# Performance work log

Hardware: AMD Instinct MI355X
Metric: run time of the kernel (lower is better)

The kernel has to match this reference:

```python
import jax, jax.numpy as jnp
import numpy as np
import math

FACTOR = 1

def setup_inputs() -> dict:
    key = jax.random.key(0)
    kq, kk, kv = jax.random.split(key, 3)
    B, H, L, E = 8, 8, 1024, 512
    queries = jax.random.normal(kq, (B, H, L, E), dtype=jnp.float32)
    keys = jax.random.normal(kk, (B, H, L, E), dtype=jnp.float32)
    values = jax.random.normal(kv, (B, H, L, E), dtype=jnp.float32)
    return {"queries": queries, "keys": keys, "values": values}

def _time_delay_agg_full(values, corr):
    # values: [B,H,C,Len], corr: [B,H,C,Len]  (C = seq positions, Len = feature dim here)
    length = values.shape[-1]
    top_k = int(FACTOR * math.log(length))
    weights, delay = jax.lax.top_k(corr, top_k)          # [B,H,C,k]
    tmp_corr = jax.nn.softmax(weights, axis=-1)          # [B,H,C,k]
    # gather from values.repeat(...,2) at init_index + delay  ==  circular gather mod length
    idx = (jnp.arange(length)[None, None, None, None, :] + delay[..., None]) % length  # [B,H,C,k,Len]
    gathered = jnp.take_along_axis(values[:, :, :, None, :], idx, axis=-1)             # [B,H,C,k,Len]
    return jnp.einsum('bhckl,bhck->bhcl', gathered, tmp_corr)

def reference(queries, keys, values):
    B, H, L, E = queries.shape
    S = values.shape[2]
    # L == S in this setup, so pad/slice branches are no-ops; keep slice for fidelity
    values = values[:, :, :L, :]
    keys = keys[:, :, :L, :]
    q_fft = jnp.fft.fft(queries, axis=-1)
    k_fft = jnp.fft.fft(keys, axis=-1)
    res = q_fft * jnp.conj(k_fft)
    # torch.fft.irfft(res, n=E) trims the complex input to E//2+1 before inverse; numpy/jax do the same
    corr = jnp.fft.irfft(res, n=E, axis=-1).astype(queries.dtype)  # [B,H,L,E]
    V = _time_delay_agg_full(values, corr)
    return V, jnp.transpose(corr, (0, 3, 1, 2))
```

## Files before the change

kernel.cpp:

```cpp
#include <hip/hip_runtime.h>
#include <math.h>


#define TOPK 6
#define LGKM0 asm volatile("s_waitcnt lgkmcnt(0)" ::: "memory")

__device__ __forceinline__ float2 cmul(float2 a, float2 b) {
  return make_float2(fmaf(a.x, b.x, -(a.y * b.y)), fmaf(a.x, b.y, a.y * b.x));
}
__device__ __forceinline__ float2 cadd(float2 a, float2 b) { return make_float2(a.x + b.x, a.y + b.y); }
__device__ __forceinline__ float2 csub(float2 a, float2 b) { return make_float2(a.x - b.x, a.y - b.y); }
__device__ __forceinline__ float2 mnegi(float2 v) { return make_float2(v.y, -v.x); }

__device__ __forceinline__ unsigned bf16rne(float x) {
  unsigned t = __float_as_uint(x);
  return (t + 0x7FFFu + ((t >> 16) & 1u)) >> 16;
}

__device__ __forceinline__ unsigned wave_umax64(unsigned x) {
#define DPPMAX(ctrl)                                                          \
  {                                                                           \
    unsigned t = (unsigned)__builtin_amdgcn_update_dpp(0, (int)x, ctrl, 0xf,  \
                                                       0xf, true);            \
    x = t > x ? t : x;                                                        \
  }
  DPPMAX(0x111)
  DPPMAX(0x112)
  DPPMAX(0x114)
  DPPMAX(0x118)
  DPPMAX(0x142)
  DPPMAX(0x143)
#undef DPPMAX
  return (unsigned)__builtin_amdgcn_readlane((int)x, 63);
}

__device__ __forceinline__ void radix8(float2 y[8]) {
  float2 p0 = cadd(y[0], y[4]), p1 = csub(y[0], y[4]);
  float2 p2 = cadd(y[2], y[6]), p3 = csub(y[2], y[6]);
  float2 q0 = cadd(y[1], y[5]), q1 = csub(y[1], y[5]);
  float2 q2 = cadd(y[3], y[7]), q3 = csub(y[3], y[7]);
  float2 mp3 = mnegi(p3), mq3 = mnegi(q3);
  float2 E0 = cadd(p0, p2), E2 = csub(p0, p2);
  float2 E1 = cadd(p1, mp3), E3 = csub(p1, mp3);
  float2 O0 = cadd(q0, q2), O2 = csub(q0, q2);
  float2 O1 = cadd(q1, mq3), O3 = csub(q1, mq3);
  const float RT = 0.70710678118654752440f;
  float2 T1 = make_float2(RT * (O1.x + O1.y), RT * (O1.y - O1.x));
  float2 T2 = mnegi(O2);
  float2 T3 = make_float2(RT * (O3.y - O3.x), -RT * (O3.x + O3.y));
  y[0] = cadd(E0, O0); y[4] = csub(E0, O0);
  y[1] = cadd(E1, T1); y[5] = csub(E1, T1);
  y[2] = cadd(E2, T2); y[6] = csub(E2, T2);
  y[3] = cadd(E3, T3); y[7] = csub(E3, T3);
}

__device__ __forceinline__ void twiddle8(float2 y[8], float2 w) {
  float2 wp = w;
  y[1] = cmul(y[1], wp);
  wp = cmul(wp, w); y[2] = cmul(y[2], wp);
  wp = cmul(wp, w); y[3] = cmul(y[3], wp);
  wp = cmul(wp, w); y[4] = cmul(y[4], wp);
  wp = cmul(wp, w); y[5] = cmul(y[5], wp);
  wp = cmul(wp, w); y[6] = cmul(y[6], wp);
  wp = cmul(wp, w); y[7] = cmul(y[7], wp);
}

__device__ __forceinline__ void fft512t(float2 y[8], float* zx, float* zy,
                                        int u, float2 w512u, float2 w64n0) {
  const int f0 = u >> 3, n0 = u & 7;
  radix8(y);
  twiddle8(y, w512u);
#pragma unroll
  for (int r = 0; r < 8; ++r) { int s = 72 * r + u; zx[s] = y[r].x; zy[s] = y[r].y; }
  LGKM0;
#pragma unroll
  for (int j = 0; j < 8; ++j) {
    int s = 72 * f0 + 8 * j + n0;
    y[j] = make_float2(zx[s], zy[s]);
  }
  radix8(y);
  twiddle8(y, w64n0);
  LGKM0;
#pragma unroll
  for (int g = 0; g < 8; ++g) {
    int s = 72 * f0 + 8 * g + (n0 ^ g);
    zx[s] = y[g].x; zy[s] = y[g].y;
  }
  LGKM0;
#pragma unroll
  for (int j = 0; j < 8; ++j) {
    int s = 72 * f0 + 8 * n0 + (j ^ n0);
    y[j] = make_float2(zx[s], zy[s]);
  }
  radix8(y);
}

__global__ __launch_bounds__(512, 4) void autoagg_kernel(
    const float* __restrict__ q, const float* __restrict__ kk,
    const float* __restrict__ v, float* __restrict__ outV,
    float* __restrict__ outC) {
  __shared__ float zscr[8 * 1152];
  __shared__ unsigned short tile[512 * 36];
  const int tid = threadIdx.x;
  const int u = tid & 63;
  const int w = tid >> 6;
  const int bid = blockIdx.x;
  float* zx = zscr + w * 1152;
  float* zy = zx + 576;

  const int f0 = u >> 3, n0 = u & 7;
  const int base = f0 + (n0 << 3);

  const float N2PI = -6.28318530717958647692f;
  float s_, c_;
  __sincosf(N2PI * (float)u * (1.f / 512.f), &s_, &c_);
  const float2 w512u = make_float2(c_, s_);
  __sincosf(N2PI * (float)n0 * (1.f / 64.f), &s_, &c_);
  const float2 w64n0 = make_float2(c_, s_);

#pragma unroll 1
  for (int p = 0; p < 4; ++p) {
    const int row = (bid << 5) + (p << 3) + w;
    const int rowU = __builtin_amdgcn_readfirstlane(row);
    const float* qrow = q + (size_t)rowU * 512;
    const float* krow = kk + (size_t)rowU * 512;
    const float* vrow = v + (size_t)rowU * 512;

    float2 y[8];
#pragma unroll
    for (int m = 0; m < 8; ++m)
      y[m] = make_float2(qrow[u + (m << 6)], krow[u + (m << 6)]);

    fft512t(y, zx, zy, u, w512u, w64n0);

    LGKM0;
#pragma unroll
    for (int r = 0; r < 8; ++r) {
      int s = 72 * r + (n0 << 3) + f0;
      zx[s] = y[r].x; zy[s] = y[r].y;
    }
    LGKM0;
    const float SCL = 1.f / 2048.f;
#pragma unroll
    for (int m = 0; m < 8; ++m) {
      int fA = (m << 6) | u;
      int fB = (512 - fA) & 511;
      int sA = 72 * m + (f0 << 3) + n0;
      int sB = 72 * (fB >> 6) + (((fB >> 3) & 7) << 3) + (fB & 7);
      float Ax = zx[sA], Ay = zy[sA];
      float Bx = zx[sB], By = zy[sB];
      float sx = Ax + Bx, sy = Ay - By;
      float dx = Ax - Bx, dy = Ay + By;
      y[m] = make_float2((sx * dy - sy * dx) * SCL,
                         -fmaf(sx, dx, sy * dy) * SCL);
    }

    fft512t(y, zx, zy, u, w512u, w64n0);

    const int col = (p << 3) | w;
#pragma unroll
    for (int r = 0; r < 8; ++r)
      tile[(base + (r << 6)) * 36 + col] = (unsigned short)bf16rne(y[r].x);

    unsigned key[8];
#pragma unroll
    for (int r = 0; r < 8; ++r) {
      unsigned bb = __float_as_uint(y[r].x);
      unsigned sgn = (unsigned)((int)bb >> 31);
      unsigned mono = bb ^ (sgn | 0x80000000u);
      key[r] = (mono & 0xFFFFFE00u) | (unsigned)(511 - (base + (r << 6)));
    }
    float w0 = 0.f, tw[TOPK]; int dly[TOPK];
#pragma unroll
    for (int it = 0; it < TOPK; ++it) {
      unsigned km = key[0];
#pragma unroll
      for (int i = 1; i < 8; ++i) km = key[i] > km ? key[i] : km;
      unsigned kmax = wave_umax64(km);
      unsigned mb = kmax & 0xFFFFFE00u;
      unsigned vb = (mb & 0x80000000u) ? (mb ^ 0x80000000u) : ~mb;
      float val = __uint_as_float(vb);
      if (it == 0) w0 = val;
      tw[it] = __expf(val - w0);
      dly[it] = 511 - (int)(kmax & 0x1FFu);
#pragma unroll
      for (int i = 0; i < 8; ++i) if (key[i] == kmax) key[i] = 0u;
    }
    float ssum = 0.f;
#pragma unroll
    for (int it = 0; it < TOPK; ++it) ssum += tw[it];
    const float inv = 1.f / ssum;

    float V[8] = {0.f, 0.f, 0.f, 0.f, 0.f, 0.f, 0.f, 0.f};
#pragma unroll
    for (int it = 0; it < TOPK; ++it) {
      const float twk = tw[it] * inv;
      const int d = dly[it];
#pragma unroll
      for (int i = 0; i < 8; ++i)
        V[i] = fmaf(twk, vrow[(base + (i << 6) + d) & 511], V[i]);
    }

    LGKM0;
#pragma unroll
    for (int i = 0; i < 8; ++i)
      zx[76 * i + 9 * n0 + f0] = V[i];
    LGKM0;
    float vt[8];
#pragma unroll
    for (int j = 0; j < 8; ++j)
      vt[j] = zx[76 * f0 + 9 * n0 + j];
    LGKM0;
    float4* ov = (float4*)(outV + (size_t)rowU * 512 + (u << 3));
    ov[0] = make_float4(vt[0], vt[1], vt[2], vt[3]);
    ov[1] = make_float4(vt[4], vt[5], vt[6], vt[7]);
  }

  __syncthreads();
  const int b9 = bid >> 8;
  const int h9 = (bid >> 5) & 7;
  const int l0 = (bid & 31) << 5;
#pragma unroll
  for (int round = 0; round < 8; ++round) {
    int e = (round << 6) + (tid >> 3);
    int lq = (tid & 7) << 2;
    const unsigned short* tr = tile + e * 36 + lq;
    float4 tv = make_float4(__uint_as_float((unsigned)tr[0] << 16),
                            __uint_as_float((unsigned)tr[1] << 16),
                            __uint_as_float((unsigned)tr[2] << 16),
                            __uint_as_float((unsigned)tr[3] << 16));
    *(float4*)(outC + (((size_t)b9 * 512 + e) * 8 + h9) * 1024 + l0 + lq) = tv;
  }
}

extern "C" void kernel_launch(void* const* d_in, const int* in_sizes, int n_in,
                              void* d_out, int out_size, void* d_ws, size_t ws_size,
                              hipStream_t stream) {
  const float* q = (const float*)d_in[0];
  const float* k = (const float*)d_in[1];
  const float* v = (const float*)d_in[2];
  float* outV = (float*)d_out;
  float* outC = (float*)d_out + (size_t)8 * 8 * 1024 * 512;
  dim3 grid(65536 / 32), block(512);
  hipLaunchKernelGGL(autoagg_kernel, grid, block, 0, stream, q, k, v, outV, outC);
}
```

Measured before the change: 230.6 us.

## Recompute twiddles in FFT, drop explicit LDS waits, raise occupancy bound

Recomputes the FFT twiddle factors inside each FFT call with __sincosf instead of keeping them live across the loop. Explicit s_waitcnt lgkmcnt(0) waits are replaced with plain compiler memory barriers. The launch bounds move from 4 to 5 blocks per CU to push register usage down. The bf16 tile readback uses one 8-byte LDS load instead of four 2-byte loads. These aim to cut register pressure and LDS wait stalls, at the cost of extra transcendental work and relying on the compiler to insert correct LDS waits within a wave.

Result: no change. 233.0 us (+1.0%).

```diff
diff --git a/kernel.cpp b/kernel.cpp
--- a/kernel.cpp
+++ b/kernel.cpp
@@ -3,7 +3,7 @@
 
 
 #define TOPK 6
-#define LGKM0 asm volatile("s_waitcnt lgkmcnt(0)" ::: "memory")
+#define CBAR asm volatile("" ::: "memory")
 
 __device__ __forceinline__ float2 cmul(float2 a, float2 b) {
   return make_float2(fmaf(a.x, b.x, -(a.y * b.y)), fmaf(a.x, b.y, a.y * b.x));
@@ -66,27 +66,31 @@
 }
 
 __device__ __forceinline__ void fft512t(float2 y[8], float* zx, float* zy,
-                                        int u, float2 w512u, float2 w64n0) {
+                                        int u) {
   const int f0 = u >> 3, n0 = u & 7;
+  const float N2PI = -6.28318530717958647692f;
+  float s_, c_;
   radix8(y);
-  twiddle8(y, w512u);
+  __sincosf(N2PI * (float)u * (1.f / 512.f), &s_, &c_);
+  twiddle8(y, make_float2(c_, s_));
 #pragma unroll
   for (int r = 0; r < 8; ++r) { int s = 72 * r + u; zx[s] = y[r].x; zy[s] = y[r].y; }
-  LGKM0;
+  CBAR;
 #pragma unroll
   for (int j = 0; j < 8; ++j) {
     int s = 72 * f0 + 8 * j + n0;
     y[j] = make_float2(zx[s], zy[s]);
   }
   radix8(y);
-  twiddle8(y, w64n0);
-  LGKM0;
+  __sincosf(N2PI * (float)n0 * (1.f / 64.f), &s_, &c_);
+  twiddle8(y, make_float2(c_, s_));
+  CBAR;
 #pragma unroll
   for (int g = 0; g < 8; ++g) {
     int s = 72 * f0 + 8 * g + (n0 ^ g);
     zx[s] = y[g].x; zy[s] = y[g].y;
   }
-  LGKM0;
+  CBAR;
 #pragma unroll
   for (int j = 0; j < 8; ++j) {
     int s = 72 * f0 + 8 * n0 + (j ^ n0);
@@ -95,7 +99,7 @@
   radix8(y);
 }
 
-__global__ __launch_bounds__(512, 4) void autoagg_kernel(
+__global__ __launch_bounds__(512, 5) void autoagg_kernel(
     const float* __restrict__ q, const float* __restrict__ kk,
     const float* __restrict__ v, float* __restrict__ outV,
     float* __restrict__ outC) {
@@ -111,13 +115,6 @@
   const int f0 = u >> 3, n0 = u & 7;
   const int base = f0 + (n0 << 3);
 
-  const float N2PI = -6.28318530717958647692f;
-  float s_, c_;
-  __sincosf(N2PI * (float)u * (1.f / 512.f), &s_, &c_);
-  const float2 w512u = make_float2(c_, s_);
-  __sincosf(N2PI * (float)n0 * (1.f / 64.f), &s_, &c_);
-  const float2 w64n0 = make_float2(c_, s_);
-
 #pragma unroll 1
   for (int p = 0; p < 4; ++p) {
     const int row = (bid << 5) + (p << 3) + w;
@@ -131,15 +128,15 @@
     for (int m = 0; m < 8; ++m)
       y[m] = make_float2(qrow[u + (m << 6)], krow[u + (m << 6)]);
 
-    fft512t(y, zx, zy, u, w512u, w64n0);
-
-    LGKM0;
+    fft512t(y, zx, zy, u);
+
+    CBAR;
 #pragma unroll
     for (int r = 0; r < 8; ++r) {
       int s = 72 * r + (n0 << 3) + f0;
       zx[s] = y[r].x; zy[s] = y[r].y;
     }
-    LGKM0;
+    CBAR;
     const float SCL = 1.f / 2048.f;
 #pragma unroll
     for (int m = 0; m < 8; ++m) {
@@ -155,7 +152,7 @@
                          -fmaf(sx, dx, sy * dy) * SCL);
     }
 
-    fft512t(y, zx, zy, u, w512u, w64n0);
+    fft512t(y, zx, zy, u);
 
     const int col = (p << 3) | w;
 #pragma unroll
@@ -201,19 +198,20 @@
         V[i] = fmaf(twk, vrow[(base + (i << 6) + d) & 511], V[i]);
     }
 
-    LGKM0;
+    CBAR;
 #pragma unroll
     for (int i = 0; i < 8; ++i)
       zx[76 * i + 9 * n0 + f0] = V[i];
-    LGKM0;
+    CBAR;
     float vt[8];
 #pragma unroll
     for (int j = 0; j < 8; ++j)
       vt[j] = zx[76 * f0 + 9 * n0 + j];
-    LGKM0;
+    CBAR;
     float4* ov = (float4*)(outV + (size_t)rowU * 512 + (u << 3));
     ov[0] = make_float4(vt[0], vt[1], vt[2], vt[3]);
     ov[1] = make_float4(vt[4], vt[5], vt[6], vt[7]);
+    CBAR;
   }
 
   __syncthreads();
@@ -224,11 +222,11 @@
   for (int round = 0; round < 8; ++round) {
     int e = (round << 6) + (tid >> 3);
     int lq = (tid & 7) << 2;
-    const unsigned short* tr = tile + e * 36 + lq;
-    float4 tv = make_float4(__uint_as_float((unsigned)tr[0] << 16),
-                            __uint_as_float((unsigned)tr[1] << 16),
-                            __uint_as_float((unsigned)tr[2] << 16),
-                            __uint_as_float((unsigned)tr[3] << 16));
+    uint2 tt = *(const uint2*)(tile + e * 36 + lq);
+    float4 tv = make_float4(__uint_as_float(tt.x << 16),
+                            __uint_as_float(tt.x & 0xFFFF0000u),
+                            __uint_as_float(tt.y << 16),
+                            __uint_as_float(tt.y & 0xFFFF0000u));
     *(float4*)(outC + (((size_t)b9 * 512 + e) * 8 + h9) * 1024 + l0 + lq) = tv;
   }
 }
```
